# Optimization experiments

Hardware: AMD Instinct MI355X
Metric: run time of the kernel (lower is better)

The kernel has to match this reference:

```python
import math
import jax, jax.numpy as jnp
import numpy as np

B, L, D, H = 4, 2048, 1024, 16
KD = D // H

def setup_inputs() -> dict:
    key = jax.random.key(0)
    k1, k2, k3 = jax.random.split(key, 3)
    x = jax.random.normal(k1, (B, L, D), dtype=jnp.float32)
    pad_mask = jnp.zeros((B, L), dtype=bool)  # True = padded (masked) key position
    w_qkv = jax.random.normal(k2, (D, 3 * D), dtype=jnp.float32) / math.sqrt(D)
    w_out = jax.random.normal(k3, (D, D), dtype=jnp.float32) / math.sqrt(D)
    return {"x": x, "pad_mask": pad_mask, "w_qkv": w_qkv, "w_out": w_out}

def reference(x, pad_mask, w_qkv, w_out):
    Bx, Lx, Dx = x.shape
    qkv = jnp.einsum('bld,de->ble', x, w_qkv)          # [B,L,3D]
    q, k, v = jnp.split(qkv, 3, axis=-1)
    def heads(t):
        return t.reshape(Bx, Lx, H, KD).transpose(0, 2, 1, 3)  # [B,H,L,kd]
    qh, kh, vh = heads(q), heads(k), heads(v)
    scores = jnp.einsum('bhqd,bhkd->bhqk', qh, kh) / math.sqrt(KD)
    causal = jnp.triu(jnp.ones((Lx, Lx), dtype=bool), k=1)[None, None]   # [1,1,L,L]
    mask = causal | pad_mask[:, None, None, :]                            # [B,1,L,L]
    scores = jnp.where(mask, -jnp.inf, scores)
    probs = jax.nn.softmax(scores, axis=-1)
    att = jnp.einsum('bhqk,bhkd->bhqd', probs, vh)
    concat = att.transpose(0, 2, 1, 3).reshape(Bx, Lx, Dx)
    return jnp.einsum('bld,de->ble', concat, w_out)
```

## Files before the change

kernel.cpp:

```cpp
#include <hip/hip_runtime.h>
#include <hip/hip_bf16.h>
#include <math.h>


typedef __bf16 bf16x8 __attribute__((ext_vector_type(8)));
typedef float f32x4 __attribute__((ext_vector_type(4)));

__device__ __forceinline__ f32x4 mfma16(bf16x8 a, bf16x8 b, f32x4 c) {
    return __builtin_amdgcn_mfma_f32_16x16x32_bf16(a, b, c, 0, 0, 0);
}

__device__ __forceinline__ void async16(const void* g, void* l) {
    __builtin_amdgcn_global_load_lds(
        (const __attribute__((address_space(1))) unsigned int*)g,
        (__attribute__((address_space(3))) unsigned int*)l, 16, 0, 0);
}

__global__ void cvt_f32_bf16_v4(const float* __restrict__ in,
                                __hip_bfloat16* __restrict__ out, int n4) {
    int i = blockIdx.x * blockDim.x + threadIdx.x;
    if (i >= n4) return;
    float4 v = ((const float4*)in)[i];
    __hip_bfloat16 t[4];
    t[0] = __float2bfloat16(v.x);
    t[1] = __float2bfloat16(v.y);
    t[2] = __float2bfloat16(v.z);
    t[3] = __float2bfloat16(v.w);
    ((uint2*)out)[i] = *(uint2*)t;
}

__global__ void transpose_cvt(const float* __restrict__ W,
                              __hip_bfloat16* __restrict__ Wt, int K, int N) {
    __shared__ float tile[32][33];
    int tid = threadIdx.x;
    int tx = tid & 31, ty = tid >> 5;
    int n0 = blockIdx.x * 32, k0 = blockIdx.y * 32;
#pragma unroll
    for (int i = 0; i < 4; ++i)
        tile[ty + 8 * i][tx] = W[(size_t)(k0 + ty + 8 * i) * N + n0 + tx];
    __syncthreads();
#pragma unroll
    for (int i = 0; i < 4; ++i)
        Wt[(size_t)(n0 + ty + 8 * i) * K + k0 + tx] =
            __float2bfloat16(tile[tx][ty + 8 * i]);
}

template <int MODE>
__global__ __launch_bounds__(256) void gemm_bf16(
    const __hip_bfloat16* __restrict__ A, const __hip_bfloat16* __restrict__ Bt,
    float* __restrict__ Cf, __hip_bfloat16* __restrict__ Qo,
    __hip_bfloat16* __restrict__ Ko, __hip_bfloat16* __restrict__ Vto, int M,
    int N, int K) {
    __shared__ __hip_bfloat16 As[128 * 64];
    __shared__ __hip_bfloat16 Bs[128 * 64];
    int tid = threadIdx.x;
    int wave = tid >> 6, lane = tid & 63;
    int quad = lane >> 4, l16 = lane & 15;
    int m0 = blockIdx.x * 128, n0 = blockIdx.y * 128;
    int wm = (wave >> 1) * 64, wn = (wave & 1) * 64;
    int srow = lane >> 3;
    int g8 = ((lane & 7) ^ srow) * 8;
    int swz = (l16 & 7);
    f32x4 acc[4][4] = {};
    for (int k0 = 0; k0 < K; k0 += 64) {
        __syncthreads();
#pragma unroll
        for (int j = 0; j < 4; ++j) {
            int r0 = (j * 4 + wave) * 8;
            async16(&A[(size_t)(m0 + r0 + srow) * K + k0 + g8], &As[r0 * 64]);
            async16(&Bt[(size_t)(n0 + r0 + srow) * K + k0 + g8], &Bs[r0 * 64]);
        }
        __syncthreads();
        bf16x8 af[2][4], bfr[2][4];
#pragma unroll
        for (int c = 0; c < 2; ++c) {
            int pg = ((c * 4 + quad) ^ swz) * 8;
#pragma unroll
            for (int i = 0; i < 4; ++i) {
                af[c][i]  = *(const bf16x8*)&As[(wm + i * 16 + l16) * 64 + pg];
                bfr[c][i] = *(const bf16x8*)&Bs[(wn + i * 16 + l16) * 64 + pg];
            }
        }
#pragma unroll
        for (int c = 0; c < 2; ++c)
#pragma unroll
            for (int mi = 0; mi < 4; ++mi)
#pragma unroll
                for (int ni = 0; ni < 4; ++ni)
                    acc[mi][ni] = mfma16(af[c][mi], bfr[c][ni], acc[mi][ni]);
    }
#pragma unroll
    for (int mi = 0; mi < 4; ++mi) {
#pragma unroll
        for (int ni = 0; ni < 4; ++ni) {
            int row0 = m0 + wm + mi * 16 + quad * 4;
            int col = n0 + wn + ni * 16 + l16;
            if (MODE == 0) {
#pragma unroll
                for (int r = 0; r < 4; ++r)
                    Cf[(size_t)(row0 + r) * N + col] = acc[mi][ni][r];
            } else {
                int which = col >> 10, hd = col & 1023;
                int h = hd >> 6, d = hd & 63;
                if (which == 0) {
#pragma unroll
                    for (int r = 0; r < 4; ++r) {
                        int row = row0 + r;
                        int b = row >> 11, l = row & 2047;
                        Qo[(((size_t)b * 16 + h) * 2048 + l) * 64 + d] =
                            __float2bfloat16(acc[mi][ni][r] * 0.18033688011f);
                    }
                } else if (which == 1) {
#pragma unroll
                    for (int r = 0; r < 4; ++r) {
                        int row = row0 + r;
                        int b = row >> 11, l = row & 2047;
                        Ko[(((size_t)b * 16 + h) * 2048 + l) * 64 + d] =
                            __float2bfloat16(acc[mi][ni][r]);
                    }
                } else {
                    int b = row0 >> 11, l = row0 & 2047;
                    __hip_bfloat16 t4[4];
#pragma unroll
                    for (int r = 0; r < 4; ++r)
                        t4[r] = __float2bfloat16(acc[mi][ni][r]);
                    *(uint2*)&Vto[(((size_t)b * 16 + h) * 64 + d) * 2048 + l] =
                        *(uint2*)t4;
                }
            }
        }
    }
}

__global__ __launch_bounds__(256, 2) void attn_kernel(
    const __hip_bfloat16* __restrict__ Q, const __hip_bfloat16* __restrict__ Kk,
    const __hip_bfloat16* __restrict__ Vt,
    const unsigned char* __restrict__ pm, __hip_bfloat16* __restrict__ Ao) {
    __shared__ __hip_bfloat16 Ks[2 * 64 * 64];
    __shared__ __hip_bfloat16 Vs[2 * 64 * 64];
    constexpr int LDK = 72;
    __shared__ __hip_bfloat16 Ps[4 * 32 * LDK];
    __shared__ unsigned char pmS[2048];
    __shared__ unsigned char pmAny[32];
    int tid = threadIdx.x;
    int wave = tid >> 6, lane = tid & 63;
    int quad = lane >> 4, l16 = lane & 15;
    int srow = lane >> 3;
    int g8 = ((lane & 7) ^ srow) * 8;
    int swz = (l16 & 7);
    int lin = blockIdx.x;
    int bh = (lin & 7) * 8 + ((lin >> 3) & 7);
    int pr = lin >> 6;
    int b = bh >> 4, h = bh & 15;
    const __hip_bfloat16* Qbh = Q + (size_t)bh * 2048 * 64;
    const __hip_bfloat16* Kbh = Kk + (size_t)bh * 2048 * 64;
    const __hip_bfloat16* Vbh = Vt + (size_t)bh * 64 * 2048;
    *(uint2*)&pmS[tid * 8] = *(const uint2*)&pm[b * 2048 + tid * 8];
    __syncthreads();
    if (tid < 32) {
        const unsigned long long* q8 = (const unsigned long long*)&pmS[tid * 64];
        unsigned long long v = q8[0] | q8[1] | q8[2] | q8[3] | q8[4] | q8[5] |
                               q8[6] | q8[7];
        pmAny[tid] = v ? 1 : 0;
    }
    __hip_bfloat16* Pw = Ps + wave * 32 * LDK;

    auto stage = [&](int kt, int buf) {
#pragma unroll
        for (int j = 0; j < 2; ++j) {
            int r0 = (j * 4 + wave) * 8;
            async16(&Kbh[((size_t)kt * 64 + r0 + srow) * 64 + g8],
                    &Ks[buf * 4096 + r0 * 64]);
            async16(&Vbh[(size_t)(r0 + srow) * 2048 + kt * 64 + g8],
                    &Vs[buf * 4096 + r0 * 64]);
        }
    };

#pragma unroll
    for (int ph = 0; ph < 2; ++ph) {
        int qt = ph ? pr : 15 - pr;
        int q0 = qt * 128;
        bf16x8 qf[2][2];
#pragma unroll
        for (int mi = 0; mi < 2; ++mi) {
            int qrow = q0 + (wave * 2 + mi) * 16 + l16;
            qf[mi][0] = *(const bf16x8*)&Qbh[(size_t)qrow * 64 + quad * 8];
            qf[mi][1] = *(const bf16x8*)&Qbh[(size_t)qrow * 64 + 32 + quad * 8];
        }
        f32x4 ov[2][4] = {};
        float lacc[2] = {};
        int ktmax = 2 * qt + 1;
        stage(0, 0);
        for (int kt = 0; kt <= ktmax; ++kt) {
            int cur = kt & 1;
            __syncthreads();
            if (kt < ktmax) stage(kt + 1, cur ^ 1);
            const __hip_bfloat16* Kc = &Ks[cur * 4096];
            const __hip_bfloat16* Vc = &Vs[cur * 4096];
            bool anyp = pmAny[kt] != 0;
            bool diag = (kt >= 2 * qt);
            float pv[2][4][4];
#pragma unroll
            for (int kn = 0; kn < 4; ++kn) {
                int krow = (kn * 16 + l16) * 64;
                bf16x8 kf0 = *(const bf16x8*)&Kc[krow + ((quad ^ swz) * 8)];
                bf16x8 kf1 = *(const bf16x8*)&Kc[krow + (((4 + quad) ^ swz) * 8)];
#pragma unroll
                for (int mi = 0; mi < 2; ++mi) {
                    f32x4 s = {};
                    s = mfma16(kf0, qf[mi][0], s);
                    s = mfma16(kf1, qf[mi][1], s);
#pragma unroll
                    for (int r = 0; r < 4; ++r)
                        pv[mi][kn][r] = __builtin_amdgcn_exp2f(s[r]);
                }
            }
            if (anyp) {
#pragma unroll
                for (int kn = 0; kn < 4; ++kn)
#pragma unroll
                    for (int r = 0; r < 4; ++r) {
                        bool pmk = pmS[kt * 64 + kn * 16 + quad * 4 + r] != 0;
#pragma unroll
                        for (int mi = 0; mi < 2; ++mi)
                            if (pmk) pv[mi][kn][r] = 0.f;
                    }
            }
            if (diag) {
#pragma unroll
                for (int mi = 0; mi < 2; ++mi) {
                    int qv = q0 + (wave * 2 + mi) * 16 + l16;
#pragma unroll
                    for (int kn = 0; kn < 4; ++kn) {
                        int key = kt * 64 + kn * 16 + quad * 4;
#pragma unroll
                        for (int r = 0; r < 4; ++r)
                            if (key + r > qv) pv[mi][kn][r] = 0.f;
                    }
                }
            }
#pragma unroll
            for (int mi = 0; mi < 2; ++mi) {
#pragma unroll
                for (int kn = 0; kn < 4; ++kn) {
                    lacc[mi] += (pv[mi][kn][0] + pv[mi][kn][1]) +
                                (pv[mi][kn][2] + pv[mi][kn][3]);
                    __hip_bfloat162 lo = __float22bfloat162_rn(
                        {pv[mi][kn][0], pv[mi][kn][1]});
                    __hip_bfloat162 hi = __float22bfloat162_rn(
                        {pv[mi][kn][2], pv[mi][kn][3]});
                    uint2 w;
                    w.x = *(unsigned int*)&lo;
                    w.y = *(unsigned int*)&hi;
                    *(uint2*)&Pw[(mi * 16 + l16) * LDK + kn * 16 + quad * 4] = w;
                }
            }
#pragma unroll
            for (int mi = 0; mi < 2; ++mi) {
#pragma unroll
                for (int hk = 0; hk < 2; ++hk) {
                    bf16x8 pf = *(const bf16x8*)&Pw[(mi * 16 + l16) * LDK +
                                                    hk * 32 + quad * 8];
#pragma unroll
                    for (int ni = 0; ni < 4; ++ni) {
                        int vrow = (ni * 16 + l16) * 64;
                        bf16x8 vf = *(const bf16x8*)&Vc[vrow +
                                                        (((hk * 4 + quad) ^ swz) *
                                                         8)];
                        ov[mi][ni] = mfma16(vf, pf, ov[mi][ni]);
                    }
                }
            }
        }
#pragma unroll
        for (int mi = 0; mi < 2; ++mi) {
            float rs = lacc[mi];
            rs += __shfl_xor(rs, 16);
            rs += __shfl_xor(rs, 32);
            float inv = 1.0f / rs;
            int qv = q0 + (wave * 2 + mi) * 16 + l16;
            size_t base = (size_t)(b * 2048 + qv) * 1024 + h * 64;
#pragma unroll
            for (int ni = 0; ni < 4; ++ni) {
                __hip_bfloat162 lo = __float22bfloat162_rn(
                    {ov[mi][ni][0] * inv, ov[mi][ni][1] * inv});
                __hip_bfloat162 hi = __float22bfloat162_rn(
                    {ov[mi][ni][2] * inv, ov[mi][ni][3] * inv});
                uint2 w;
                w.x = *(unsigned int*)&lo;
                w.y = *(unsigned int*)&hi;
                *(uint2*)&Ao[base + ni * 16 + quad * 4] = w;
            }
        }
        lacc[0] = lacc[1] = 0.f;
    }
}

extern "C" void kernel_launch(void* const* d_in, const int* in_sizes, int n_in,
                              void* d_out, int out_size, void* d_ws,
                              size_t ws_size, hipStream_t stream) {
    (void)in_sizes; (void)n_in; (void)out_size; (void)ws_size;
    const float* x = (const float*)d_in[0];
    const unsigned char* pm = (const unsigned char*)d_in[1];
    const float* wqkv = (const float*)d_in[2];
    const float* wout = (const float*)d_in[3];
    float* out = (float*)d_out;

    char* p = (char*)d_ws;
    auto alloc = [&](size_t bytes) {
        char* q = p;
        p += (bytes + 255) & ~(size_t)255;
        return q;
    };
    __hip_bfloat16* xb    = (__hip_bfloat16*)alloc((size_t)8192 * 1024 * 2);
    __hip_bfloat16* wqkvT = (__hip_bfloat16*)alloc((size_t)3072 * 1024 * 2);
    __hip_bfloat16* woutT = (__hip_bfloat16*)alloc((size_t)1024 * 1024 * 2);
    __hip_bfloat16* qws   = (__hip_bfloat16*)alloc((size_t)8192 * 1024 * 2);
    __hip_bfloat16* kws   = (__hip_bfloat16*)alloc((size_t)8192 * 1024 * 2);
    __hip_bfloat16* vtws  = (__hip_bfloat16*)alloc((size_t)8192 * 1024 * 2);
    __hip_bfloat16* attb  = (__hip_bfloat16*)alloc((size_t)8192 * 1024 * 2);

    cvt_f32_bf16_v4<<<8192, 256, 0, stream>>>(x, xb, 8192 * 1024 / 4);
    transpose_cvt<<<dim3(3072 / 32, 1024 / 32), 256, 0, stream>>>(wqkv, wqkvT,
                                                                  1024, 3072);
    transpose_cvt<<<dim3(1024 / 32, 1024 / 32), 256, 0, stream>>>(wout, woutT,
                                                                  1024, 1024);
    gemm_bf16<1><<<dim3(64, 24), 256, 0, stream>>>(xb, wqkvT, nullptr, qws, kws,
                                                   vtws, 8192, 3072, 1024);
    attn_kernel<<<512, 256, 0, stream>>>(qws, kws, vtws, pm, attb);
    gemm_bf16<0><<<dim3(64, 8), 256, 0, stream>>>(attb, woutT, out, nullptr,
                                                  nullptr, nullptr, 8192, 1024,
                                                  1024);
}
```

Baseline: 239.3 us.

## Split attention into one q-tile per block and split-K the output GEMM

The attention kernel now handles a single 128-row query tile per block instead of a paired long/short tile. That doubles the grid to 1024 blocks and removes the K/V double buffer, cutting LDS use so four blocks fit per CU. The q-tile index mapping interleaves long and short tiles to balance load. The output projection GEMM is split along K into two halves that accumulate into the output with float atomics, which needs a memset first. The costs are lost load/compute overlap in attention, unbalanced per-block work, atomic traffic, and nondeterministic summation order.

```diff
diff --git a/kernel.cpp b/kernel.cpp
--- a/kernel.cpp
+++ b/kernel.cpp
@@ -61,8 +61,14 @@
     int srow = lane >> 3;
     int g8 = ((lane & 7) ^ srow) * 8;
     int swz = (l16 & 7);
+    int kbeg = 0, kend = K;
+    if (MODE == 2) {
+        int kh = K >> 1;
+        kbeg = blockIdx.z * kh;
+        kend = kbeg + kh;
+    }
     f32x4 acc[4][4] = {};
-    for (int k0 = 0; k0 < K; k0 += 64) {
+    for (int k0 = kbeg; k0 < kend; k0 += 64) {
         __syncthreads();
 #pragma unroll
         for (int j = 0; j < 4; ++j) {
@@ -99,6 +105,11 @@
 #pragma unroll
                 for (int r = 0; r < 4; ++r)
                     Cf[(size_t)(row0 + r) * N + col] = acc[mi][ni][r];
+            } else if (MODE == 2) {
+#pragma unroll
+                for (int r = 0; r < 4; ++r)
+                    atomicAdd(&Cf[(size_t)(row0 + r) * N + col],
+                              acc[mi][ni][r]);
             } else {
                 int which = col >> 10, hd = col & 1023;
                 int h = hd >> 6, d = hd & 63;
@@ -132,12 +143,12 @@
     }
 }
 
-__global__ __launch_bounds__(256, 2) void attn_kernel(
+__global__ __launch_bounds__(256, 4) void attn_kernel(
     const __hip_bfloat16* __restrict__ Q, const __hip_bfloat16* __restrict__ Kk,
     const __hip_bfloat16* __restrict__ Vt,
     const unsigned char* __restrict__ pm, __hip_bfloat16* __restrict__ Ao) {
-    __shared__ __hip_bfloat16 Ks[2 * 64 * 64];
-    __shared__ __hip_bfloat16 Vs[2 * 64 * 64];
+    __shared__ __hip_bfloat16 Ks[64 * 64];
+    __shared__ __hip_bfloat16 Vs[64 * 64];
     constexpr int LDK = 72;
     __shared__ __hip_bfloat16 Ps[4 * 32 * LDK];
     __shared__ unsigned char pmS[2048];
@@ -150,7 +161,9 @@
     int swz = (l16 & 7);
     int lin = blockIdx.x;
     int bh = (lin & 7) * 8 + ((lin >> 3) & 7);
-    int pr = lin >> 6;
+    int raw = lin >> 6;
+    int base = (raw & 3) * 2 + (raw >> 3);
+    int qt = ((raw >> 2) & 1) ? 15 - base : base;
     int b = bh >> 4, h = bh & 15;
     const __hip_bfloat16* Qbh = Q + (size_t)bh * 2048 * 64;
     const __hip_bfloat16* Kbh = Kk + (size_t)bh * 2048 * 64;
@@ -164,135 +177,120 @@
         pmAny[tid] = v ? 1 : 0;
     }
     __hip_bfloat16* Pw = Ps + wave * 32 * LDK;
-
-    auto stage = [&](int kt, int buf) {
+    int q0 = qt * 128;
+    bf16x8 qf[2][2];
+#pragma unroll
+    for (int mi = 0; mi < 2; ++mi) {
+        int qrow = q0 + (wave * 2 + mi) * 16 + l16;
+        qf[mi][0] = *(const bf16x8*)&Qbh[(size_t)qrow * 64 + quad * 8];
+        qf[mi][1] = *(const bf16x8*)&Qbh[(size_t)qrow * 64 + 32 + quad * 8];
+    }
+    f32x4 ov[2][4] = {};
+    float lacc[2] = {};
+    int ktmax = 2 * qt + 1;
+    for (int kt = 0; kt <= ktmax; ++kt) {
+        __syncthreads();
 #pragma unroll
         for (int j = 0; j < 2; ++j) {
             int r0 = (j * 4 + wave) * 8;
-            async16(&Kbh[((size_t)kt * 64 + r0 + srow) * 64 + g8],
-                    &Ks[buf * 4096 + r0 * 64]);
+            async16(&Kbh[((size_t)kt * 64 + r0 + srow) * 64 + g8], &Ks[r0 * 64]);
             async16(&Vbh[(size_t)(r0 + srow) * 2048 + kt * 64 + g8],
-                    &Vs[buf * 4096 + r0 * 64]);
-        }
-    };
-
-#pragma unroll
-    for (int ph = 0; ph < 2; ++ph) {
-        int qt = ph ? pr : 15 - pr;
-        int q0 = qt * 128;
-        bf16x8 qf[2][2];
+                    &Vs[r0 * 64]);
+        }
+        __syncthreads();
+        bool anyp = pmAny[kt] != 0;
+        bool diag = (kt >= 2 * qt);
+        float pv[2][4][4];
+#pragma unroll
+        for (int kn = 0; kn < 4; ++kn) {
+            int krow = (kn * 16 + l16) * 64;
+            bf16x8 kf0 = *(const bf16x8*)&Ks[krow + ((quad ^ swz) * 8)];
+            bf16x8 kf1 = *(const bf16x8*)&Ks[krow + (((4 + quad) ^ swz) * 8)];
+#pragma unroll
+            for (int mi = 0; mi < 2; ++mi) {
+                f32x4 s = {};
+                s = mfma16(kf0, qf[mi][0], s);
+                s = mfma16(kf1, qf[mi][1], s);
+#pragma unroll
+                for (int r = 0; r < 4; ++r)
+                    pv[mi][kn][r] = __builtin_amdgcn_exp2f(s[r]);
+            }
+        }
+        if (anyp) {
+#pragma unroll
+            for (int kn = 0; kn < 4; ++kn)
+#pragma unroll
+                for (int r = 0; r < 4; ++r) {
+                    bool pmk = pmS[kt * 64 + kn * 16 + quad * 4 + r] != 0;
+#pragma unroll
+                    for (int mi = 0; mi < 2; ++mi)
+                        if (pmk) pv[mi][kn][r] = 0.f;
+                }
+        }
+        if (diag) {
+#pragma unroll
+            for (int mi = 0; mi < 2; ++mi) {
+                int qv = q0 + (wave * 2 + mi) * 16 + l16;
+#pragma unroll
+                for (int kn = 0; kn < 4; ++kn) {
+                    int key = kt * 64 + kn * 16 + quad * 4;
+#pragma unroll
+                    for (int r = 0; r < 4; ++r)
+                        if (key + r > qv) pv[mi][kn][r] = 0.f;
+                }
+            }
+        }
 #pragma unroll
         for (int mi = 0; mi < 2; ++mi) {
-            int qrow = q0 + (wave * 2 + mi) * 16 + l16;
-            qf[mi][0] = *(const bf16x8*)&Qbh[(size_t)qrow * 64 + quad * 8];
-            qf[mi][1] = *(const bf16x8*)&Qbh[(size_t)qrow * 64 + 32 + quad * 8];
-        }
-        f32x4 ov[2][4] = {};
-        float lacc[2] = {};
-        int ktmax = 2 * qt + 1;
-        stage(0, 0);
-        for (int kt = 0; kt <= ktmax; ++kt) {
-            int cur = kt & 1;
-            __syncthreads();
-            if (kt < ktmax) stage(kt + 1, cur ^ 1);
-            const __hip_bfloat16* Kc = &Ks[cur * 4096];
-            const __hip_bfloat16* Vc = &Vs[cur * 4096];
-            bool anyp = pmAny[kt] != 0;
-            bool diag = (kt >= 2 * qt);
-            float pv[2][4][4];
 #pragma unroll
             for (int kn = 0; kn < 4; ++kn) {
-                int krow = (kn * 16 + l16) * 64;
-                bf16x8 kf0 = *(const bf16x8*)&Kc[krow + ((quad ^ swz) * 8)];
-                bf16x8 kf1 = *(const bf16x8*)&Kc[krow + (((4 + quad) ^ swz) * 8)];
-#pragma unroll
-                for (int mi = 0; mi < 2; ++mi) {
-                    f32x4 s = {};
-                    s = mfma16(kf0, qf[mi][0], s);
-                    s = mfma16(kf1, qf[mi][1], s);
-#pragma unroll
-                    for (int r = 0; r < 4; ++r)
-                        pv[mi][kn][r] = __builtin_amdgcn_exp2f(s[r]);
-                }
-            }
-            if (anyp) {
-#pragma unroll
-                for (int kn = 0; kn < 4; ++kn)
-#pragma unroll
-                    for (int r = 0; r < 4; ++r) {
-                        bool pmk = pmS[kt * 64 + kn * 16 + quad * 4 + r] != 0;
-#pragma unroll
-                        for (int mi = 0; mi < 2; ++mi)
-                            if (pmk) pv[mi][kn][r] = 0.f;
-                    }
-            }
-            if (diag) {
-#pragma unroll
-                for (int mi = 0; mi < 2; ++mi) {
-                    int qv = q0 + (wave * 2 + mi) * 16 + l16;
-#pragma unroll
-                    for (int kn = 0; kn < 4; ++kn) {
-                        int key = kt * 64 + kn * 16 + quad * 4;
-#pragma unroll
-                        for (int r = 0; r < 4; ++r)
-                            if (key + r > qv) pv[mi][kn][r] = 0.f;
-                    }
-                }
-            }
-#pragma unroll
-            for (int mi = 0; mi < 2; ++mi) {
-#pragma unroll
-                for (int kn = 0; kn < 4; ++kn) {
-                    lacc[mi] += (pv[mi][kn][0] + pv[mi][kn][1]) +
-                                (pv[mi][kn][2] + pv[mi][kn][3]);
-                    __hip_bfloat162 lo = __float22bfloat162_rn(
-                        {pv[mi][kn][0], pv[mi][kn][1]});
-                    __hip_bfloat162 hi = __float22bfloat162_rn(
-                        {pv[mi][kn][2], pv[mi][kn][3]});
-                    uint2 w;
-                    w.x = *(unsigned int*)&lo;
-                    w.y = *(unsigned int*)&hi;
-                    *(uint2*)&Pw[(mi * 16 + l16) * LDK + kn * 16 + quad * 4] = w;
-                }
-            }
-#pragma unroll
-            for (int mi = 0; mi < 2; ++mi) {
-#pragma unroll
-                for (int hk = 0; hk < 2; ++hk) {
-                    bf16x8 pf = *(const bf16x8*)&Pw[(mi * 16 + l16) * LDK +
-                                                    hk * 32 + quad * 8];
-#pragma unroll
-                    for (int ni = 0; ni < 4; ++ni) {
-                        int vrow = (ni * 16 + l16) * 64;
-                        bf16x8 vf = *(const bf16x8*)&Vc[vrow +
-                                                        (((hk * 4 + quad) ^ swz) *
-                                                         8)];
-                        ov[mi][ni] = mfma16(vf, pf, ov[mi][ni]);
-                    }
-                }
-            }
-        }
-#pragma unroll
-        for (int mi = 0; mi < 2; ++mi) {
-            float rs = lacc[mi];
-            rs += __shfl_xor(rs, 16);
-            rs += __shfl_xor(rs, 32);
-            float inv = 1.0f / rs;
-            int qv = q0 + (wave * 2 + mi) * 16 + l16;
-            size_t base = (size_t)(b * 2048 + qv) * 1024 + h * 64;
-#pragma unroll
-            for (int ni = 0; ni < 4; ++ni) {
-                __hip_bfloat162 lo = __float22bfloat162_rn(
-                    {ov[mi][ni][0] * inv, ov[mi][ni][1] * inv});
-                __hip_bfloat162 hi = __float22bfloat162_rn(
-                    {ov[mi][ni][2] * inv, ov[mi][ni][3] * inv});
+                lacc[mi] += (pv[mi][kn][0] + pv[mi][kn][1]) +
+                            (pv[mi][kn][2] + pv[mi][kn][3]);
+                __hip_bfloat162 lo =
+                    __float22bfloat162_rn({pv[mi][kn][0], pv[mi][kn][1]});
+                __hip_bfloat162 hi =
+                    __float22bfloat162_rn({pv[mi][kn][2], pv[mi][kn][3]});
                 uint2 w;
                 w.x = *(unsigned int*)&lo;
                 w.y = *(unsigned int*)&hi;
-                *(uint2*)&Ao[base + ni * 16 + quad * 4] = w;
-            }
-        }
-        lacc[0] = lacc[1] = 0.f;
+                *(uint2*)&Pw[(mi * 16 + l16) * LDK + kn * 16 + quad * 4] = w;
+            }
+        }
+#pragma unroll
+        for (int mi = 0; mi < 2; ++mi) {
+#pragma unroll
+            for (int hk = 0; hk < 2; ++hk) {
+                bf16x8 pf = *(const bf16x8*)&Pw[(mi * 16 + l16) * LDK +
+                                                hk * 32 + quad * 8];
+#pragma unroll
+                for (int ni = 0; ni < 4; ++ni) {
+                    int vrow = (ni * 16 + l16) * 64;
+                    bf16x8 vf =
+                        *(const bf16x8*)&Vs[vrow + (((hk * 4 + quad) ^ swz) * 8)];
+                    ov[mi][ni] = mfma16(vf, pf, ov[mi][ni]);
+                }
+            }
+        }
+    }
+#pragma unroll
+    for (int mi = 0; mi < 2; ++mi) {
+        float rs = lacc[mi];
+        rs += __shfl_xor(rs, 16);
+        rs += __shfl_xor(rs, 32);
+        float inv = 1.0f / rs;
+        int qv = q0 + (wave * 2 + mi) * 16 + l16;
+        size_t obase = (size_t)(b * 2048 + qv) * 1024 + h * 64;
+#pragma unroll
+        for (int ni = 0; ni < 4; ++ni) {
+            __hip_bfloat162 lo = __float22bfloat162_rn(
+                {ov[mi][ni][0] * inv, ov[mi][ni][1] * inv});
+            __hip_bfloat162 hi = __float22bfloat162_rn(
+                {ov[mi][ni][2] * inv, ov[mi][ni][3] * inv});
+            uint2 w;
+            w.x = *(unsigned int*)&lo;
+            w.y = *(unsigned int*)&hi;
+            *(uint2*)&Ao[obase + ni * 16 + quad * 4] = w;
+        }
     }
 }
 
@@ -320,6 +318,7 @@
     __hip_bfloat16* vtws  = (__hip_bfloat16*)alloc((size_t)8192 * 1024 * 2);
     __hip_bfloat16* attb  = (__hip_bfloat16*)alloc((size_t)8192 * 1024 * 2);
 
+    hipMemsetAsync(out, 0, (size_t)8192 * 1024 * 4, stream);
     cvt_f32_bf16_v4<<<8192, 256, 0, stream>>>(x, xb, 8192 * 1024 / 4);
     transpose_cvt<<<dim3(3072 / 32, 1024 / 32), 256, 0, stream>>>(wqkv, wqkvT,
                                                                   1024, 3072);
@@ -327,8 +326,8 @@
                                                                   1024, 1024);
     gemm_bf16<1><<<dim3(64, 24), 256, 0, stream>>>(xb, wqkvT, nullptr, qws, kws,
                                                    vtws, 8192, 3072, 1024);
-    attn_kernel<<<512, 256, 0, stream>>>(qws, kws, vtws, pm, attb);
-    gemm_bf16<0><<<dim3(64, 8), 256, 0, stream>>>(attb, woutT, out, nullptr,
-                                                  nullptr, nullptr, 8192, 1024,
-                                                  1024);
-}
+    attn_kernel<<<1024, 256, 0, stream>>>(qws, kws, vtws, pm, attb);
+    gemm_bf16<2><<<dim3(64, 8, 2), 256, 0, stream>>>(attb, woutT, out, nullptr,
+                                                     nullptr, nullptr, 8192,
+                                                     1024, 1024);
+}
```

After: 289.2 us. 1.21x slower.
